# Kernel tuning notes

Measured on AMD Instinct MI355X. Metric: run time of the kernel, lower is better.

Reference implementation:

```python
import jax, jax.numpy as jnp
import numpy as np

B, S, V, D, H = 8, 256, 32000, 1024, 1024
NLAY_H, NLAY_L, HEADS = 2, 2, 8
RATIO, N_LOW, N_HIGH = 4, 16, 4
HD = H // HEADS


def setup_inputs():
    key = jax.random.key(0)
    ks = jax.random.split(key, 16)
    s = 0.02
    f = lambda k, shape: (jax.random.normal(k, shape) * s).astype(jnp.float32)
    return {
        "input_ids": jax.random.randint(ks[0], (B, S), 0, V),
        "emb": f(ks[1], (V, D)),
        "pos": f(ks[2], (S, D)),
        "Wih_h": f(ks[3], (NLAY_H, 3 * H, H)),
        "bih_h": jnp.zeros((NLAY_H, 3 * H), jnp.float32),
        "Whh_h": f(ks[4], (NLAY_H, 3 * H, H)),
        "bhh_h": jnp.zeros((NLAY_H, 3 * H), jnp.float32),
        "Win": f(ks[5], (H, 2 * H)),
        "bin_": jnp.zeros((H,), jnp.float32),
        "Wq": f(ks[6], (H, H)),
        "Wk": f(ks[7], (H, H)),
        "Wv": f(ks[8], (H, H)),
        "Wo": f(ks[9], (H, H)),
        "Wih_l": f(ks[10], (NLAY_L, 3 * H, H)),
        "bih_l": jnp.zeros((NLAY_L, 3 * H), jnp.float32),
        "Whh_l": f(ks[11], (NLAY_L, 3 * H, H)),
        "bhh_l": jnp.zeros((NLAY_L, 3 * H), jnp.float32),
        "ln_g": jnp.ones((H,), jnp.float32),
        "ln_b": jnp.zeros((H,), jnp.float32),
        "Wout": f(ks[12], (V, H)),
    }


def gru_cell(x, h, Wih, bih, Whh, bhh):
    gx = x @ Wih.T + bih  # [B, 3H]
    gh = h @ Whh.T + bhh
    xr, xz, xn = jnp.split(gx, 3, axis=-1)
    hr, hz, hn = jnp.split(gh, 3, axis=-1)
    r = jax.nn.sigmoid(xr + hr)
    z = jax.nn.sigmoid(xz + hz)
    n = jnp.tanh(xn + r * hn)
    return (1.0 - z) * n + z * h


def _forward(input_ids, emb, pos, Wih_h, bih_h, Whh_h, bhh_h, Win, bin_,
             Wq, Wk, Wv, Wo, Wih_l, bih_l, Whh_l, bhh_l, ln_g, ln_b, Wout):
    embeds = emb[input_ids] + pos[None, :S]  # [B, S, D]
    inv_sqrt_hd = np.float32(1.0 / np.sqrt(HD))

    def high_mod(x, hs):  # hs: [NLAY_H, B, H]
        new = []
        for l in range(NLAY_H):
            x = gru_cell(x, hs[l], Wih_h[l], bih_h[l], Whh_h[l], bhh_h[l])
            new.append(x)
        return jnp.stack(new), x

    def low_mod(x, high_cur, hist, mask, ls):
        # input projection over [embed ; current high state]
        inp = jax.nn.gelu(jnp.concatenate([x, high_cur], axis=-1) @ Win.T + bin_)  # [B, H]
        # multi-head cross-attention over high-state history (causal in high steps)
        q = (inp @ Wq.T).reshape(B, HEADS, HD)
        k = (hist @ Wk.T).reshape(B, N_HIGH, HEADS, HD)
        v = (hist @ Wv.T).reshape(B, N_HIGH, HEADS, HD)
        scores = jnp.einsum('bhd,bthd->bht', q, k) * inv_sqrt_hd
        scores = jnp.where(mask[None, None, :], scores, jnp.float32(-1e9))
        attn = jax.nn.softmax(scores, axis=-1)
        ctx = jnp.einsum('bht,bthd->bhd', attn, v).reshape(B, H) @ Wo.T
        x2 = inp + ctx
        new = []
        for l in range(NLAY_L):
            x2 = gru_cell(x2, ls[l], Wih_l[l], bih_l[l], Whh_l[l], bhh_l[l])
            new.append(x2)
        return jnp.stack(new), x2

    def step(carry, t):
        hs_all, ls_all, hist = carry
        e = embeds[:, t]  # [B, D]
        low_step = t % N_LOW
        high_step = low_step // RATIO
        do_high = (low_step % RATIO) == 0
        hs = hs_all[high_step]
        new_hs, high_out = high_mod(e, hs)
        hs_all = hs_all.at[high_step].set(jnp.where(do_high, new_hs, hs))
        hist = hist.at[:, high_step].set(jnp.where(do_high, high_out, hist[:, high_step]))
        mask = jnp.arange(N_HIGH) <= high_step
        ls = ls_all[low_step]
        new_ls, low_out = low_mod(e, hist[:, high_step], hist, mask, ls)
        ls_all = ls_all.at[low_step].set(new_ls)
        mu = low_out.mean(axis=-1, keepdims=True)
        var = ((low_out - mu) ** 2).mean(axis=-1, keepdims=True)
        y = (low_out - mu) / jnp.sqrt(var + 1e-5) * ln_g + ln_b
        return (hs_all, ls_all, hist), y @ Wout.T  # [B, V]

    hs0 = jnp.zeros((N_HIGH, NLAY_H, B, H), jnp.float32)
    ls0 = jnp.zeros((N_LOW, NLAY_L, B, H), jnp.float32)
    hist0 = jnp.zeros((B, N_HIGH, H), jnp.float32)
    _, logits = jax.lax.scan(step, (hs0, ls0, hist0), jnp.arange(S))
    return jnp.transpose(logits, (1, 0, 2))  # [B, S, V]


def reference(input_ids, emb, pos, Wih_h, bih_h, Whh_h, bhh_h, Win, bin_,
              Wq, Wk, Wv, Wo, Wih_l, bih_l, Whh_l, bhh_l, ln_g, ln_b, Wout):
    return _forward(input_ids, emb, pos, Wih_h, bih_h, Whh_h, bhh_h, Win, bin_,
                    Wq, Wk, Wv, Wo, Wih_l, bih_l, Whh_l, bhh_l, ln_g, ln_b, Wout)
```

## Files before the change

kernel.cpp:

```cpp
#include <hip/hip_runtime.h>

typedef unsigned short u16;
typedef float f32x4 __attribute__((ext_vector_type(4)));
typedef __bf16 bf16x8 __attribute__((ext_vector_type(8)));
typedef u16 u16x8 __attribute__((ext_vector_type(8)));

#define DEVFN __device__ __forceinline__


DEVFN u16 f2bf(float f) {
  unsigned u = __builtin_bit_cast(unsigned, f);
  unsigned r = u + 0x7FFFu + ((u >> 16) & 1u);
  return (u16)(r >> 16);
}

DEVFN bf16x8 cvt8(const float* p) {
  float4 f0 = *reinterpret_cast<const float4*>(p);
  float4 f1 = *reinterpret_cast<const float4*>(p + 4);
  u16x8 u;
  u[0] = f2bf(f0.x); u[1] = f2bf(f0.y); u[2] = f2bf(f0.z); u[3] = f2bf(f0.w);
  u[4] = f2bf(f1.x); u[5] = f2bf(f1.y); u[6] = f2bf(f1.z); u[7] = f2bf(f1.w);
  return __builtin_bit_cast(bf16x8, u);
}

DEVFN bf16x8 ldbf(const u16* p) { return *reinterpret_cast<const bf16x8*>(p); }
DEVFN float sigm(float x) { return 1.f / (1.f + expf(-x)); }

DEVFN void gload16(const u16* g, u16* l) {
  __builtin_amdgcn_global_load_lds(
      (const __attribute__((address_space(1))) void*)g,
      (__attribute__((address_space(3))) void*)l, 16, 0, 0);
}

template<int NTSTORE, int OUTF, int BF16OUT, int CADD>
__global__ __launch_bounds__(256) void gemm_lds(
    const u16* __restrict__ A, const u16* __restrict__ W,
    const float* __restrict__ Cadd,
    float* __restrict__ OUT, u16* __restrict__ OUTbf,
    int ldo, int mtiles) {
  __shared__ u16 smA[2][128 * 32];
  __shared__ u16 smB[2][128 * 32];

  int nwg = gridDim.x;
  int orig = blockIdx.x;
  int q = nwg >> 3, r = nwg & 7;
  int xcd = orig & 7, idx = orig >> 3;
  int wg = (xcd < r ? xcd * (q + 1) : r * (q + 1) + (xcd - r) * q) + idx;
  int m0 = (wg % mtiles) * 128;
  int n0 = (wg / mtiles) * 128;

  int tid = threadIdx.x;
  int wv = tid >> 6, lane = tid & 63;
  int lrow = lane >> 2;
  int gcol = ((lane & 3) ^ (lrow & 3)) << 3;

  const u16* gA0 = A + (size_t)(m0 + wv * 32 + lrow) * 1024 + gcol;
  const u16* gB0 = W + (size_t)(n0 + wv * 32 + lrow) * 1024 + gcol;
  u16* lA0 = &smA[0][(wv * 32) * 32];
  u16* lA1 = &smA[0][(wv * 32 + 16) * 32];
  u16* lB0 = &smB[0][(wv * 32) * 32];
  u16* lB1 = &smB[0][(wv * 32 + 16) * 32];
  const int BUFO = 128 * 32;

  f32x4 acc[4][4];
#pragma unroll
  for (int mi = 0; mi < 4; ++mi)
#pragma unroll
    for (int ni = 0; ni < 4; ++ni) acc[mi][ni] = f32x4{0.f, 0.f, 0.f, 0.f};

  int qm = (wv >> 1) * 64, qn = (wv & 1) * 64;
  int lr = lane & 15;
  int kk = (lane >> 4) << 3;

  gload16(gA0, lA0);
  gload16(gA0 + 16 * 1024, lA1);
  gload16(gB0, lB0);
  gload16(gB0 + 16 * 1024, lB1);

  for (int kt = 0; kt < 32; ++kt) {
    int buf = kt & 1;
    __syncthreads();
    if (kt < 31) {
      int k0 = (kt + 1) << 5;
      int bo = (buf ^ 1) * BUFO;
      gload16(gA0 + k0, lA0 + bo);
      gload16(gA0 + 16 * 1024 + k0, lA1 + bo);
      gload16(gB0 + k0, lB0 + bo);
      gload16(gB0 + 16 * 1024 + k0, lB1 + bo);
    }
    bf16x8 av[4], bv[4];
#pragma unroll
    for (int i = 0; i < 4; ++i) {
      int ra = qm + i * 16 + lr;
      av[i] = *(const bf16x8*)&smA[buf][ra * 32 + (kk ^ ((ra & 3) << 3))];
      int rbw = qn + i * 16 + lr;
      bv[i] = *(const bf16x8*)&smB[buf][rbw * 32 + (kk ^ ((rbw & 3) << 3))];
    }
#pragma unroll
    for (int mi = 0; mi < 4; ++mi)
#pragma unroll
      for (int ni = 0; ni < 4; ++ni)
        acc[mi][ni] = __builtin_amdgcn_mfma_f32_16x16x32_bf16(av[mi], bv[ni], acc[mi][ni], 0, 0, 0);
  }

  int rb = (lane >> 4) << 2;
#pragma unroll
  for (int mi = 0; mi < 4; ++mi)
#pragma unroll
    for (int ni = 0; ni < 4; ++ni)
#pragma unroll
      for (int rr = 0; rr < 4; ++rr) {
        int row = m0 + qm + mi * 16 + rb + rr;
        int col = n0 + qn + ni * 16 + lr;
        size_t o = (size_t)row * (size_t)ldo + col;
        float v = acc[mi][ni][rr];
        if constexpr (CADD) v += Cadd[o];
        if constexpr (OUTF) {
          if constexpr (NTSTORE) __builtin_nontemporal_store(v, &OUT[o]);
          else OUT[o] = v;
        }
        if constexpr (BF16OUT) OUTbf[o] = f2bf(v);
      }
}

template<int MT, int NT, int KW>
__global__ __launch_bounds__(64 * KW) void gemm2(
    const u16* __restrict__ A, int lda,
    const void* __restrict__ Wp, int ldw, int kwoff, int wbf,
    const float* __restrict__ Cadd, int ldc,
    float* __restrict__ OUT, u16* __restrict__ OUTbf, int ldo, int K) {
  int tid = threadIdx.x;
  int kw = tid >> 6;
  int lane = tid & 63;
  int lr = lane & 15;
  int kk = (lane >> 4) << 3;
  int n0 = blockIdx.x * (16 * NT);
  int m0 = blockIdx.y * (16 * MT);
  int KP = K / KW;
  int kb = kw * KP + kk;

  f32x4 acc[MT][NT];
#pragma unroll
  for (int mi = 0; mi < MT; ++mi)
#pragma unroll
    for (int ni = 0; ni < NT; ++ni) acc[mi][ni] = f32x4{0.f, 0.f, 0.f, 0.f};

  const u16* ap[MT];
#pragma unroll
  for (int mi = 0; mi < MT; ++mi) ap[mi] = A + (size_t)(m0 + mi * 16 + lr) * (size_t)lda + kb;

  if (wbf) {
    const u16* wb[NT];
#pragma unroll
    for (int ni = 0; ni < NT; ++ni)
      wb[ni] = (const u16*)Wp + (size_t)(n0 + ni * 16 + lr) * (size_t)ldw + kwoff + kb;
    for (int k0 = 0; k0 < KP; k0 += 32) {
      bf16x8 wv[NT];
#pragma unroll
      for (int ni = 0; ni < NT; ++ni) wv[ni] = ldbf(wb[ni] + k0);
#pragma unroll
      for (int mi = 0; mi < MT; ++mi) {
        bf16x8 a = ldbf(ap[mi] + k0);
#pragma unroll
        for (int ni = 0; ni < NT; ++ni)
          acc[mi][ni] = __builtin_amdgcn_mfma_f32_16x16x32_bf16(a, wv[ni], acc[mi][ni], 0, 0, 0);
      }
    }
  } else {
    const float* wf[NT];
#pragma unroll
    for (int ni = 0; ni < NT; ++ni)
      wf[ni] = (const float*)Wp + (size_t)(n0 + ni * 16 + lr) * (size_t)ldw + kwoff + kb;
    for (int k0 = 0; k0 < KP; k0 += 32) {
      bf16x8 wv[NT];
#pragma unroll
      for (int ni = 0; ni < NT; ++ni) wv[ni] = cvt8(wf[ni] + k0);
#pragma unroll
      for (int mi = 0; mi < MT; ++mi) {
        bf16x8 a = ldbf(ap[mi] + k0);
#pragma unroll
        for (int ni = 0; ni < NT; ++ni)
          acc[mi][ni] = __builtin_amdgcn_mfma_f32_16x16x32_bf16(a, wv[ni], acc[mi][ni], 0, 0, 0);
      }
    }
  }

  if constexpr (KW > 1) {
    __shared__ f32x4 red[KW][MT * NT][64];
#pragma unroll
    for (int mi = 0; mi < MT; ++mi)
#pragma unroll
      for (int ni = 0; ni < NT; ++ni) red[kw][mi * NT + ni][lane] = acc[mi][ni];
    __syncthreads();
    if (kw) return;
    for (int w2 = 1; w2 < KW; ++w2)
#pragma unroll
      for (int mi = 0; mi < MT; ++mi)
#pragma unroll
        for (int ni = 0; ni < NT; ++ni) acc[mi][ni] += red[w2][mi * NT + ni][lane];
  }

  int rb = (lane >> 4) << 2;
#pragma unroll
  for (int mi = 0; mi < MT; ++mi)
#pragma unroll
    for (int ni = 0; ni < NT; ++ni)
#pragma unroll
      for (int rr = 0; rr < 4; ++rr) {
        int row = m0 + mi * 16 + rb + rr;
        int col = n0 + ni * 16 + lr;
        size_t o = (size_t)row * (size_t)ldo + col;
        float v = acc[mi][ni][rr];
        if (Cadd) v += Cadd[(size_t)row * (size_t)ldc + col];
        if (OUT) OUT[o] = v;
        if (OUTbf) OUTbf[o] = f2bf(v);
      }
}

struct GruP {
  const u16* X; const u16* Hb; const float* Hf;
  const u16* Wbih; const u16* Wbhh;
  const float* Wfih; const float* Wfhh;
  const float* bih; const float* bhh;
  float* Hof; u16* Hob; u16* hist;
};

__global__ __launch_bounds__(256) void gru_dual(GruP pa, GruP pb, int tiles1, int wbf) {
  GruP p; int m0;
  if ((int)blockIdx.y < tiles1) { p = pa; m0 = blockIdx.y * 32; }
  else { p = pb; m0 = ((int)blockIdx.y - tiles1) * 32; }
  int tid = threadIdx.x;
  int kw = tid >> 6;
  int lane = tid & 63;
  int lr = lane & 15;
  int kk = (lane >> 4) << 3;
  int j0 = blockIdx.x * 16;
  const int KP = 256;
  int kb = kw * KP + kk;

  f32x4 aR[2], aZ[2], aNX[2], aNH[2];
#pragma unroll
  for (int mi = 0; mi < 2; ++mi) {
    aR[mi] = f32x4{0.f, 0.f, 0.f, 0.f};
    aZ[mi] = f32x4{0.f, 0.f, 0.f, 0.f};
    aNX[mi] = f32x4{0.f, 0.f, 0.f, 0.f};
    aNH[mi] = f32x4{0.f, 0.f, 0.f, 0.f};
  }

  const u16* xp[2];
  const u16* hp[2];
#pragma unroll
  for (int mi = 0; mi < 2; ++mi) {
    size_t ro = (size_t)(m0 + mi * 16 + lr) * 1024 + kb;
    xp[mi] = p.X + ro;
    hp[mi] = p.Hb + ro;
  }

  size_t wro = (size_t)(j0 + lr) * 1024 + kb;
  if (wbf) {
    const u16 *pxr = p.Wbih + wro, *pxz = p.Wbih + wro + 1048576, *pxn = p.Wbih + wro + 2097152;
    const u16 *phr = p.Wbhh + wro, *phz = p.Wbhh + wro + 1048576, *phn = p.Wbhh + wro + 2097152;
    for (int k0 = 0; k0 < KP; k0 += 32) {
      bf16x8 wxr = ldbf(pxr + k0), wxz = ldbf(pxz + k0), wxn = ldbf(pxn + k0);
      bf16x8 whr = ldbf(phr + k0), whz = ldbf(phz + k0), whn = ldbf(phn + k0);
#pragma unroll
      for (int mi = 0; mi < 2; ++mi) {
        bf16x8 ax = ldbf(xp[mi] + k0);
        bf16x8 ah = ldbf(hp[mi] + k0);
        aR[mi] = __builtin_amdgcn_mfma_f32_16x16x32_bf16(ax, wxr, aR[mi], 0, 0, 0);
        aR[mi] = __builtin_amdgcn_mfma_f32_16x16x32_bf16(ah, whr, aR[mi], 0, 0, 0);
        aZ[mi] = __builtin_amdgcn_mfma_f32_16x16x32_bf16(ax, wxz, aZ[mi], 0, 0, 0);
        aZ[mi] = __builtin_amdgcn_mfma_f32_16x16x32_bf16(ah, whz, aZ[mi], 0, 0, 0);
        aNX[mi] = __builtin_amdgcn_mfma_f32_16x16x32_bf16(ax, wxn, aNX[mi], 0, 0, 0);
        aNH[mi] = __builtin_amdgcn_mfma_f32_16x16x32_bf16(ah, whn, aNH[mi], 0, 0, 0);
      }
    }
  } else {
    const float *pxr = p.Wfih + wro, *pxz = p.Wfih + wro + 1048576, *pxn = p.Wfih + wro + 2097152;
    const float *phr = p.Wfhh + wro, *phz = p.Wfhh + wro + 1048576, *phn = p.Wfhh + wro + 2097152;
    for (int k0 = 0; k0 < KP; k0 += 32) {
      bf16x8 wxr = cvt8(pxr + k0), wxz = cvt8(pxz + k0), wxn = cvt8(pxn + k0);
      bf16x8 whr = cvt8(phr + k0), whz = cvt8(phz + k0), whn = cvt8(phn + k0);
#pragma unroll
      for (int mi = 0; mi < 2; ++mi) {
        bf16x8 ax = ldbf(xp[mi] + k0);
        bf16x8 ah = ldbf(hp[mi] + k0);
        aR[mi] = __builtin_amdgcn_mfma_f32_16x16x32_bf16(ax, wxr, aR[mi], 0, 0, 0);
        aR[mi] = __builtin_amdgcn_mfma_f32_16x16x32_bf16(ah, whr, aR[mi], 0, 0, 0);
        aZ[mi] = __builtin_amdgcn_mfma_f32_16x16x32_bf16(ax, wxz, aZ[mi], 0, 0, 0);
        aZ[mi] = __builtin_amdgcn_mfma_f32_16x16x32_bf16(ah, whz, aZ[mi], 0, 0, 0);
        aNX[mi] = __builtin_amdgcn_mfma_f32_16x16x32_bf16(ax, wxn, aNX[mi], 0, 0, 0);
        aNH[mi] = __builtin_amdgcn_mfma_f32_16x16x32_bf16(ah, whn, aNH[mi], 0, 0, 0);
      }
    }
  }

  {
    __shared__ f32x4 red[4][8][64];
#pragma unroll
    for (int mi = 0; mi < 2; ++mi) {
      red[kw][mi * 4 + 0][lane] = aR[mi];
      red[kw][mi * 4 + 1][lane] = aZ[mi];
      red[kw][mi * 4 + 2][lane] = aNX[mi];
      red[kw][mi * 4 + 3][lane] = aNH[mi];
    }
    __syncthreads();
    if (kw) return;
    for (int w2 = 1; w2 < 4; ++w2)
#pragma unroll
      for (int mi = 0; mi < 2; ++mi) {
        aR[mi] += red[w2][mi * 4 + 0][lane];
        aZ[mi] += red[w2][mi * 4 + 1][lane];
        aNX[mi] += red[w2][mi * 4 + 2][lane];
        aNH[mi] += red[w2][mi * 4 + 3][lane];
      }
  }

  int c = j0 + lr;
  float br = p.bih[c] + p.bhh[c];
  float bz = p.bih[1024 + c] + p.bhh[1024 + c];
  float bnx = p.bih[2048 + c];
  float bnh = p.bhh[2048 + c];
  int rb = (lane >> 4) << 2;
#pragma unroll
  for (int mi = 0; mi < 2; ++mi)
#pragma unroll
    for (int rr = 0; rr < 4; ++rr) {
      int row = m0 + mi * 16 + rb + rr;
      float r = sigm(aR[mi][rr] + br);
      float z = sigm(aZ[mi][rr] + bz);
      float n = tanhf(aNX[mi][rr] + bnx + r * (aNH[mi][rr] + bnh));
      size_t o = (size_t)row * 1024 + c;
      float hv = (1.f - z) * n + z * p.Hf[o];
      p.Hof[o] = hv;
      u16 hb = f2bf(hv);
      p.Hob[o] = hb;
      if (p.hist) p.hist[o] = hb;
    }
}

__global__ __launch_bounds__(256) void gemm_big(const u16* __restrict__ A,
                                                const void* __restrict__ Wp, int wbf,
                                                float* __restrict__ OUT) {
  int wv = threadIdx.x >> 6;
  int lane = threadIdx.x & 63;
  int lr = lane & 15;
  int kk = (lane >> 4) << 3;
  int m0 = blockIdx.x * 256 + wv * 64;
  int n0 = blockIdx.y * 64;

  f32x4 acc[4][4];
#pragma unroll
  for (int mi = 0; mi < 4; ++mi)
#pragma unroll
    for (int ni = 0; ni < 4; ++ni) acc[mi][ni] = f32x4{0.f, 0.f, 0.f, 0.f};

  const u16* ap[4];
#pragma unroll
  for (int mi = 0; mi < 4; ++mi) ap[mi] = A + (size_t)(m0 + mi * 16 + lr) * 1024 + kk;

  const float* wf[4];
#pragma unroll
  for (int ni = 0; ni < 4; ++ni) wf[ni] = (const float*)Wp + (size_t)(n0 + ni * 16 + lr) * 1024 + kk;
  for (int k0 = 0; k0 < 1024; k0 += 32) {
    bf16x8 wvv[4];
#pragma unroll
    for (int ni = 0; ni < 4; ++ni) wvv[ni] = cvt8(wf[ni] + k0);
#pragma unroll
    for (int mi = 0; mi < 4; ++mi) {
      bf16x8 a = ldbf(ap[mi] + k0);
#pragma unroll
      for (int ni = 0; ni < 4; ++ni)
        acc[mi][ni] = __builtin_amdgcn_mfma_f32_16x16x32_bf16(a, wvv[ni], acc[mi][ni], 0, 0, 0);
    }
  }

  int rb = (lane >> 4) << 2;
#pragma unroll
  for (int mi = 0; mi < 4; ++mi)
#pragma unroll
    for (int ni = 0; ni < 4; ++ni)
#pragma unroll
      for (int rr = 0; rr < 4; ++rr) {
        size_t o = (size_t)(m0 + mi * 16 + rb + rr) * 32000 + (size_t)(n0 + ni * 16 + lr);
        __builtin_nontemporal_store(acc[mi][ni][rr], &OUT[o]);
      }
}

__global__ void cvt_w(const float* __restrict__ src, int src_ld, int col_off,
                      u16* __restrict__ dst, int log2c) {
  size_t idx = ((size_t)blockIdx.x * 256 + threadIdx.x) * 8;
  size_t row = idx >> log2c;
  int col = (int)(idx & ((1u << log2c) - 1));
  const float* s = src + row * (size_t)src_ld + col_off + col;
  *reinterpret_cast<u16x8*>(dst + idx) = __builtin_bit_cast(u16x8, cvt8(s));
}

__global__ void embed_kernel(const int* __restrict__ ids, const float* __restrict__ emb,
                             const float* __restrict__ pos, u16* __restrict__ out) {
  int idx = blockIdx.x * 256 + threadIdx.x;
  int e8 = (idx & 127) << 3;
  int rb = idx >> 7;
  int t = rb >> 3, b = rb & 7;
  int w = t >> 4, lsp = t & 15, g = lsp >> 2, o = lsp & 3;
  int R = ((w << 4) + (o << 2) + g) * 8 + b;
  int tok = ids[b * 256 + t];
  const float* ep = emb + (size_t)tok * 1024 + e8;
  const float* pp = pos + (size_t)t * 1024 + e8;
  u16x8 u;
#pragma unroll
  for (int i = 0; i < 8; ++i) u[i] = f2bf(ep[i] + pp[i]);
  *reinterpret_cast<u16x8*>(out + (size_t)R * 1024 + e8) = u;
}

__global__ void inp_all(const float* __restrict__ einp, const float* __restrict__ kvhAll,
                        const float* __restrict__ bin, float* __restrict__ inpb,
                        u16* __restrict__ inpbf) {
  int idx = blockIdx.x * 256 + threadIdx.x;
  int r = idx >> 10, j = idx & 1023;
  int w = r >> 7, r7 = r & 127;
  int g = (r7 >> 3) & 3, b = r7 & 7;
  float x = einp[idx] + kvhAll[(size_t)(w * 32 + g * 8 + b) * 3072 + 2048 + j] + bin[j];
  float t = tanhf(0.7978845608028654f * (x + 0.044715f * x * x * x));
  float v = 0.5f * x * (1.f + t);
  inpb[idx] = v;
  inpbf[idx] = f2bf(v);
}

__global__ void attn_all(const float* __restrict__ qb, const float* __restrict__ kvhAll,
                         u16* __restrict__ ctxbf) {
  int r = blockIdx.x;
  int w = r >> 7, r7 = r & 127;
  int sp = r7 >> 3;
  int g = sp & 3;
  int b = r7 & 7;
  int lane = threadIdx.x;
  const float* kvb = kvhAll + (size_t)w * 32 * 3072;
  __shared__ float aw[8][4];
  if (lane < 32) {
    int head = lane >> 2, t = lane & 3;
    float s = 0.f;
    if (t <= g) {
      const float* qp = qb + (size_t)r * 1024 + head * 128;
      const float* kp = kvb + (size_t)(t * 8 + b) * 3072 + head * 128;
      for (int d = 0; d < 128; ++d) s += qp[d] * kp[d];
      s *= 0.08838834764831845f;
    }
    float sc[4];
    sc[0] = __shfl(s, (head << 2) + 0);
    sc[1] = __shfl(s, (head << 2) + 1);
    sc[2] = __shfl(s, (head << 2) + 2);
    sc[3] = __shfl(s, (head << 2) + 3);
    if (t == 0) {
      float mx = -1e30f;
      for (int u = 0; u <= g; ++u) mx = fmaxf(mx, sc[u]);
      float p[4] = {0.f, 0.f, 0.f, 0.f};
      float den = 0.f;
      for (int u = 0; u <= g; ++u) { p[u] = expf(sc[u] - mx); den += p[u]; }
      float inv = 1.f / den;
      for (int u = 0; u < 4; ++u) aw[head][u] = (u <= g) ? p[u] * inv : 0.f;
    }
  }
  __syncthreads();
  for (int idx = lane; idx < 1024; idx += 64) {
    int head = idx >> 7;
    float acc = 0.f;
#pragma unroll
    for (int t = 0; t < 4; ++t) acc += aw[head][t] * kvb[(size_t)(t * 8 + b) * 3072 + 1024 + idx];
    ctxbf[(size_t)r * 1024 + idx] = f2bf(acc);
  }
}

__global__ void ln_all(const float* __restrict__ ls1f, const float* __restrict__ g_,
                       const float* __restrict__ b_, u16* __restrict__ Ybf) {
  int bid = blockIdx.x;
  int w = bid >> 7, r7 = bid & 127;
  int tid = threadIdx.x;
  const float* x = ls1f + (size_t)(w + 1) * 131072 + (size_t)r7 * 1024;
  float s = 0.f, s2 = 0.f;
  for (int j = tid; j < 1024; j += 256) { float v = x[j]; s += v; s2 += v * v; }
  for (int off = 32; off; off >>= 1) { s += __shfl_xor(s, off); s2 += __shfl_xor(s2, off); }
  __shared__ float rs[4], rs2[4], mv[2];
  int wv = tid >> 6;
  if ((tid & 63) == 0) { rs[wv] = s; rs2[wv] = s2; }
  __syncthreads();
  if (tid == 0) {
    float S = rs[0] + rs[1] + rs[2] + rs[3];
    float S2 = rs2[0] + rs2[1] + rs2[2] + rs2[3];
    float mu = S * (1.f / 1024.f);
    float var = S2 * (1.f / 1024.f) - mu * mu;
    mv[0] = mu;
    mv[1] = rsqrtf(var + 1e-5f);
  }
  __syncthreads();
  float mu = mv[0], rstd = mv[1];
  int sp = r7 >> 3, b = r7 & 7;
  int g = sp & 3, o = sp >> 2;
  int t = w * 16 + g * 4 + o;
  u16* yrow = Ybf + (size_t)(b * 256 + t) * 1024;
  for (int j = tid; j < 1024; j += 256) {
    float v = (x[j] - mu) * rstd * g_[j] + b_[j];
    yrow[j] = f2bf(v);
  }
}

extern "C" void kernel_launch(void* const* d_in, const int* in_sizes, int n_in,
                              void* d_out, int out_size, void* d_ws, size_t ws_size,
                              hipStream_t stream) {
  const int* ids = (const int*)d_in[0];
  const float* emb = (const float*)d_in[1];
  const float* pos = (const float*)d_in[2];
  const float* Wih_h = (const float*)d_in[3];
  const float* bih_h = (const float*)d_in[4];
  const float* Whh_h = (const float*)d_in[5];
  const float* bhh_h = (const float*)d_in[6];
  const float* Win = (const float*)d_in[7];
  const float* bin_ = (const float*)d_in[8];
  const float* Wq = (const float*)d_in[9];
  const float* Wk = (const float*)d_in[10];
  const float* Wv = (const float*)d_in[11];
  const float* Wo = (const float*)d_in[12];
  const float* Wih_l = (const float*)d_in[13];
  const float* bih_l = (const float*)d_in[14];
  const float* Whh_l = (const float*)d_in[15];
  const float* bhh_l = (const float*)d_in[16];
  const float* ln_g = (const float*)d_in[17];
  const float* ln_b = (const float*)d_in[18];
  const float* Wout = (const float*)d_in[19];
  float* out = (float*)d_out;

  size_t off = 0;
  char* wsb = (char*)d_ws;
  auto allocF = [&](size_t n) { float* p = (float*)(wsb + off); off += n * 4; return p; };
  auto allocU = [&](size_t n) { u16* p = (u16*)(wsb + off); off += n * 2; return p; };

  float* hs0f = allocF((size_t)17 * 32768);
  float* hs1f = allocF((size_t)17 * 32768);
  float* ls0f = allocF((size_t)17 * 131072);
  float* ls1f = allocF((size_t)17 * 131072);
  u16* hs0b = allocU((size_t)17 * 32768);
  u16* hs1b = allocU((size_t)17 * 32768);
  u16* ls0b = allocU((size_t)17 * 131072);
  u16* ls1b = allocU((size_t)17 * 131072);
  u16* histAll = allocU(524288);
  u16* embB = allocU(2097152);
  float* einp = allocF(2097152);
  float* kvhAll = allocF((size_t)512 * 3072);
  float* inpb = allocF(2097152);
  u16* inpbf = allocU(2097152);
  float* qb = allocF(2097152);
  u16* ctxbf = allocU(2097152);
  u16* x2bf = allocU(2097152);
  u16* Ybf = allocU(2097152);

  const size_t WPACK_BYTES = (size_t)(4 * 6291456 + 1048576 + 1048576 + 1048576 + 3145728) * 2;
  bool packW = (off + WPACK_BYTES <= ws_size);
  u16 *WihHb = nullptr, *WhhHb = nullptr, *WihLb = nullptr, *WhhLb = nullptr;
  u16 *WinB0 = nullptr, *WqB = nullptr, *WoB = nullptr, *KVp = nullptr;
  if (packW) {
    WihHb = allocU(6291456);
    WhhHb = allocU(6291456);
    WihLb = allocU(6291456);
    WhhLb = allocU(6291456);
    WinB0 = allocU(1048576);
    WqB = allocU(1048576);
    WoB = allocU(1048576);
    KVp = allocU(3145728);
  }
  bool packWout = packW && (off + (size_t)32768000 * 2 <= ws_size);
  u16* WoutB = nullptr;
  if (packWout) WoutB = allocU(32768000);

  (void)hipMemsetAsync(hs0f, 0, 32768 * 4, stream);
  (void)hipMemsetAsync(hs1f, 0, 32768 * 4, stream);
  (void)hipMemsetAsync(ls0f, 0, 131072 * 4, stream);
  (void)hipMemsetAsync(ls1f, 0, 131072 * 4, stream);
  (void)hipMemsetAsync(hs0b, 0, 32768 * 2, stream);
  (void)hipMemsetAsync(hs1b, 0, 32768 * 2, stream);
  (void)hipMemsetAsync(ls0b, 0, 131072 * 2, stream);
  (void)hipMemsetAsync(ls1b, 0, 131072 * 2, stream);

  embed_kernel<<<1024, 256, 0, stream>>>(ids, emb, pos, embB);
  if (packW) {
    cvt_w<<<3072, 256, 0, stream>>>(Wih_h, 1024, 0, WihHb, 10);
    cvt_w<<<3072, 256, 0, stream>>>(Whh_h, 1024, 0, WhhHb, 10);
    cvt_w<<<3072, 256, 0, stream>>>(Wih_l, 1024, 0, WihLb, 10);
    cvt_w<<<3072, 256, 0, stream>>>(Whh_l, 1024, 0, WhhLb, 10);
    cvt_w<<<512, 256, 0, stream>>>(Win, 2048, 0, WinB0, 10);
    cvt_w<<<512, 256, 0, stream>>>(Wq, 1024, 0, WqB, 10);
    cvt_w<<<512, 256, 0, stream>>>(Wo, 1024, 0, WoB, 10);
    cvt_w<<<512, 256, 0, stream>>>(Wk, 1024, 0, KVp, 10);
    cvt_w<<<512, 256, 0, stream>>>(Wv, 1024, 0, KVp + 1048576, 10);
    cvt_w<<<512, 256, 0, stream>>>(Win, 2048, 1024, KVp + 2097152, 10);
  }
  if (packWout) cvt_w<<<16000, 256, 0, stream>>>(Wout, 1024, 0, WoutB, 10);
  int wbfW = packW ? 1 : 0;

  if (packW)
    gemm_lds<0, 1, 0, 0><<<128, 256, 0, stream>>>(embB, WinB0, nullptr, einp, nullptr, 1024, 16);
  else
    gemm2<2, 2, 2><<<dim3(32, 64), 128, 0, stream>>>(
        embB, 1024, Win, 2048, 0, 0, nullptr, 0, einp, nullptr, 1024, 1024);

  const size_t LW = (size_t)3072 * 1024;
  auto HP = [&](int layer, int w) {
    GruP p;
    if (layer == 0) {
      p.X = embB + (size_t)w * 131072;
      p.Hb = hs0b + (size_t)w * 32768; p.Hf = hs0f + (size_t)w * 32768;
      p.Wbih = WihHb; p.Wbhh = WhhHb; p.Wfih = Wih_h; p.Wfhh = Whh_h;
      p.bih = bih_h; p.bhh = bhh_h;
      p.Hof = hs0f + (size_t)(w + 1) * 32768; p.Hob = hs0b + (size_t)(w + 1) * 32768;
      p.hist = nullptr;
    } else {
      p.X = hs0b + (size_t)(w + 1) * 32768;
      p.Hb = hs1b + (size_t)w * 32768; p.Hf = hs1f + (size_t)w * 32768;
      p.Wbih = WihHb ? WihHb + LW : nullptr; p.Wbhh = WhhHb ? WhhHb + LW : nullptr;
      p.Wfih = Wih_h + LW; p.Wfhh = Whh_h + LW;
      p.bih = bih_h + 3072; p.bhh = bhh_h + 3072;
      p.Hof = hs1f + (size_t)(w + 1) * 32768; p.Hob = hs1b + (size_t)(w + 1) * 32768;
      p.hist = histAll + (size_t)w * 32768;
    }
    return p;
  };
  auto LP = [&](int layer, int w) {
    GruP p;
    if (layer == 0) {
      p.X = x2bf + (size_t)w * 131072;
      p.Hb = ls0b + (size_t)w * 131072; p.Hf = ls0f + (size_t)w * 131072;
      p.Wbih = WihLb; p.Wbhh = WhhLb; p.Wfih = Wih_l; p.Wfhh = Whh_l;
      p.bih = bih_l; p.bhh = bhh_l;
      p.Hof = ls0f + (size_t)(w + 1) * 131072; p.Hob = ls0b + (size_t)(w + 1) * 131072;
      p.hist = nullptr;
    } else {
      p.X = ls0b + (size_t)(w + 1) * 131072;
      p.Hb = ls1b + (size_t)w * 131072; p.Hf = ls1f + (size_t)w * 131072;
      p.Wbih = WihLb ? WihLb + LW : nullptr; p.Wbhh = WhhLb ? WhhLb + LW : nullptr;
      p.Wfih = Wih_l + LW; p.Wfhh = Whh_l + LW;
      p.bih = bih_l + 3072; p.bhh = bhh_l + 3072;
      p.Hof = ls1f + (size_t)(w + 1) * 131072; p.Hob = ls1b + (size_t)(w + 1) * 131072;
      p.hist = nullptr;
    }
    return p;
  };

  gru_dual<<<dim3(64, 1), 256, 0, stream>>>(HP(0, 0), HP(0, 0), 1, wbfW);
  for (int d = 1; d <= 15; ++d)
    gru_dual<<<dim3(64, 2), 256, 0, stream>>>(HP(1, d - 1), HP(0, d), 1, wbfW);
  gru_dual<<<dim3(64, 1), 256, 0, stream>>>(HP(1, 15), HP(1, 15), 1, wbfW);

  if (packW) {
    gemm_lds<0, 1, 0, 0><<<96, 256, 0, stream>>>(histAll, KVp, nullptr, kvhAll, nullptr, 3072, 4);
  } else {
    gemm2<2, 2, 2><<<dim3(32, 16), 128, 0, stream>>>(
        histAll, 1024, Wk, 1024, 0, 0, nullptr, 0, kvhAll, nullptr, 3072, 1024);
    gemm2<2, 2, 2><<<dim3(32, 16), 128, 0, stream>>>(
        histAll, 1024, Wv, 1024, 0, 0, nullptr, 0, kvhAll + 1024, nullptr, 3072, 1024);
    gemm2<2, 2, 2><<<dim3(32, 16), 128, 0, stream>>>(
        histAll, 1024, Win, 2048, 1024, 0, nullptr, 0, kvhAll + 2048, nullptr, 3072, 1024);
  }
  inp_all<<<8192, 256, 0, stream>>>(einp, kvhAll, bin_, inpb, inpbf);
  if (packW)
    gemm_lds<0, 1, 0, 0><<<128, 256, 0, stream>>>(inpbf, WqB, nullptr, qb, nullptr, 1024, 16);
  else
    gemm2<2, 2, 2><<<dim3(32, 64), 128, 0, stream>>>(
        inpbf, 1024, Wq, 1024, 0, 0, nullptr, 0, qb, nullptr, 1024, 1024);
  attn_all<<<2048, 64, 0, stream>>>(qb, kvhAll, ctxbf);
  if (packW)
    gemm_lds<0, 0, 1, 1><<<128, 256, 0, stream>>>(ctxbf, WoB, inpb, nullptr, x2bf, 1024, 16);
  else
    gemm2<2, 2, 2><<<dim3(32, 64), 128, 0, stream>>>(
        ctxbf, 1024, Wo, 1024, 0, 0, inpb, 1024, nullptr, x2bf, 1024, 1024);

  gru_dual<<<dim3(64, 4), 256, 0, stream>>>(LP(0, 0), LP(0, 0), 4, wbfW);
  for (int d = 1; d <= 15; ++d)
    gru_dual<<<dim3(64, 8), 256, 0, stream>>>(LP(1, d - 1), LP(0, d), 4, wbfW);
  gru_dual<<<dim3(64, 4), 256, 0, stream>>>(LP(1, 15), LP(1, 15), 4, wbfW);

  ln_all<<<2048, 256, 0, stream>>>(ls1f, ln_g, ln_b, Ybf);
  if (packWout)
    gemm_lds<1, 1, 0, 0><<<4000, 256, 0, stream>>>(Ybf, WoutB, nullptr, out, nullptr, 32000, 16);
  else
    gemm_big<<<dim3(8, 500), 256, 0, stream>>>(Ybf, Wout, 0, out);
}
```

Measured before the change: 1.109 ms.

## Merge weight conversion launches into one kernel and retune GEMM LDS swizzle

Replaces eleven separate fp32-to-bf16 weight conversion launches with a single segmented kernel that finds its segment from the block index, removing per-launch overhead and tail gaps. Separately, the LDS tile swizzle in the bf16 GEMM now XORs on row bits 1-2 instead of 0-1, and the per-iteration shared-memory read offsets are precomputed outside the k-loop. The swizzle change is meant to reduce LDS bank conflicts on the fragment reads. The segment search adds a small serial loop per block.

Measured after the change: 1.081 ms. 2.5% less time.

```diff
diff --git a/kernel.cpp b/kernel.cpp
--- a/kernel.cpp
+++ b/kernel.cpp
@@ -52,10 +52,10 @@
   int tid = threadIdx.x;
   int wv = tid >> 6, lane = tid & 63;
   int lrow = lane >> 2;
-  int gcol = ((lane & 3) ^ (lrow & 3)) << 3;
-
-  const u16* gA0 = A + (size_t)(m0 + wv * 32 + lrow) * 1024 + gcol;
-  const u16* gB0 = W + (size_t)(n0 + wv * 32 + lrow) * 1024 + gcol;
+  int gcol = ((lane & 3) ^ ((lrow >> 1) & 3)) << 3;
+
+  const u16* gA = A + (size_t)(m0 + wv * 32 + lrow) * 1024 + gcol;
+  const u16* gB = W + (size_t)(n0 + wv * 32 + lrow) * 1024 + gcol;
   u16* lA0 = &smA[0][(wv * 32) * 32];
   u16* lA1 = &smA[0][(wv * 32 + 16) * 32];
   u16* lB0 = &smB[0][(wv * 32) * 32];
@@ -72,10 +72,21 @@
   int lr = lane & 15;
   int kk = (lane >> 4) << 3;
 
-  gload16(gA0, lA0);
-  gload16(gA0 + 16 * 1024, lA1);
-  gload16(gB0, lB0);
-  gload16(gB0 + 16 * 1024, lB1);
+  int offA[4], offB[4];
+#pragma unroll
+  for (int i = 0; i < 4; ++i) {
+    int ra = qm + i * 16 + lr;
+    offA[i] = ra * 64 + ((kk ^ (((ra >> 1) & 3) << 3)) << 1);
+    int rbw = qn + i * 16 + lr;
+    offB[i] = rbw * 64 + ((kk ^ (((rbw >> 1) & 3) << 3)) << 1);
+  }
+  const char* baseA = (const char*)&smA[0][0];
+  const char* baseB = (const char*)&smB[0][0];
+
+  gload16(gA, lA0);
+  gload16(gA + 16 * 1024, lA1);
+  gload16(gB, lB0);
+  gload16(gB + 16 * 1024, lB1);
 
   for (int kt = 0; kt < 32; ++kt) {
     int buf = kt & 1;
@@ -83,18 +94,17 @@
     if (kt < 31) {
       int k0 = (kt + 1) << 5;
       int bo = (buf ^ 1) * BUFO;
-      gload16(gA0 + k0, lA0 + bo);
-      gload16(gA0 + 16 * 1024 + k0, lA1 + bo);
-      gload16(gB0 + k0, lB0 + bo);
-      gload16(gB0 + 16 * 1024 + k0, lB1 + bo);
-    }
+      gload16(gA + k0, lA0 + bo);
+      gload16(gA + 16 * 1024 + k0, lA1 + bo);
+      gload16(gB + k0, lB0 + bo);
+      gload16(gB + 16 * 1024 + k0, lB1 + bo);
+    }
+    int bb = buf * (BUFO * 2);
     bf16x8 av[4], bv[4];
 #pragma unroll
     for (int i = 0; i < 4; ++i) {
-      int ra = qm + i * 16 + lr;
-      av[i] = *(const bf16x8*)&smA[buf][ra * 32 + (kk ^ ((ra & 3) << 3))];
-      int rbw = qn + i * 16 + lr;
-      bv[i] = *(const bf16x8*)&smB[buf][rbw * 32 + (kk ^ ((rbw & 3) << 3))];
+      av[i] = *(const bf16x8*)(baseA + bb + offA[i]);
+      bv[i] = *(const bf16x8*)(baseB + bb + offB[i]);
     }
 #pragma unroll
     for (int mi = 0; mi < 4; ++mi)
@@ -387,13 +397,19 @@
       }
 }
 
-__global__ void cvt_w(const float* __restrict__ src, int src_ld, int col_off,
-                      u16* __restrict__ dst, int log2c) {
-  size_t idx = ((size_t)blockIdx.x * 256 + threadIdx.x) * 8;
-  size_t row = idx >> log2c;
-  int col = (int)(idx & ((1u << log2c) - 1));
-  const float* s = src + row * (size_t)src_ld + col_off + col;
-  *reinterpret_cast<u16x8*>(dst + idx) = __builtin_bit_cast(u16x8, cvt8(s));
+struct CvtSeg { const float* src; u16* dst; int src_ld; int col_off; int log2c; int nblk; };
+struct CvtArgs { CvtSeg seg[11]; int nseg; };
+
+__global__ void cvt_all(CvtArgs a) {
+  int blk = blockIdx.x;
+  int s = 0;
+  while (s < a.nseg - 1 && blk >= a.seg[s].nblk) { blk -= a.seg[s].nblk; ++s; }
+  const CvtSeg g = a.seg[s];
+  size_t idx = ((size_t)blk * 256 + threadIdx.x) * 8;
+  size_t row = idx >> g.log2c;
+  int col = (int)(idx & ((1u << g.log2c) - 1));
+  const float* sp = g.src + row * (size_t)g.src_ld + g.col_off + col;
+  *reinterpret_cast<u16x8*>(g.dst + idx) = __builtin_bit_cast(u16x8, cvt8(sp));
 }
 
 __global__ void embed_kernel(const int* __restrict__ ids, const float* __restrict__ emb,
@@ -582,18 +598,27 @@
 
   embed_kernel<<<1024, 256, 0, stream>>>(ids, emb, pos, embB);
   if (packW) {
-    cvt_w<<<3072, 256, 0, stream>>>(Wih_h, 1024, 0, WihHb, 10);
-    cvt_w<<<3072, 256, 0, stream>>>(Whh_h, 1024, 0, WhhHb, 10);
-    cvt_w<<<3072, 256, 0, stream>>>(Wih_l, 1024, 0, WihLb, 10);
-    cvt_w<<<3072, 256, 0, stream>>>(Whh_l, 1024, 0, WhhLb, 10);
-    cvt_w<<<512, 256, 0, stream>>>(Win, 2048, 0, WinB0, 10);
-    cvt_w<<<512, 256, 0, stream>>>(Wq, 1024, 0, WqB, 10);
-    cvt_w<<<512, 256, 0, stream>>>(Wo, 1024, 0, WoB, 10);
-    cvt_w<<<512, 256, 0, stream>>>(Wk, 1024, 0, KVp, 10);
-    cvt_w<<<512, 256, 0, stream>>>(Wv, 1024, 0, KVp + 1048576, 10);
-    cvt_w<<<512, 256, 0, stream>>>(Win, 2048, 1024, KVp + 2097152, 10);
-  }
-  if (packWout) cvt_w<<<16000, 256, 0, stream>>>(Wout, 1024, 0, WoutB, 10);
+    CvtArgs ca{};
+    int ns = 0, tot = 0;
+    auto add = [&](const float* s, u16* d, int ld, int co, int l2c, size_t nelem) {
+      int nb = (int)(nelem / 2048);
+      ca.seg[ns++] = CvtSeg{s, d, ld, co, l2c, nb};
+      tot += nb;
+    };
+    add(Wih_h, WihHb, 1024, 0, 10, 6291456);
+    add(Whh_h, WhhHb, 1024, 0, 10, 6291456);
+    add(Wih_l, WihLb, 1024, 0, 10, 6291456);
+    add(Whh_l, WhhLb, 1024, 0, 10, 6291456);
+    add(Win, WinB0, 2048, 0, 10, 1048576);
+    add(Wq, WqB, 1024, 0, 10, 1048576);
+    add(Wo, WoB, 1024, 0, 10, 1048576);
+    add(Wk, KVp, 1024, 0, 10, 1048576);
+    add(Wv, KVp + 1048576, 1024, 0, 10, 1048576);
+    add(Win, KVp + 2097152, 2048, 1024, 10, 1048576);
+    if (packWout) add(Wout, WoutB, 1024, 0, 10, 32768000);
+    ca.nseg = ns;
+    cvt_all<<<tot, 256, 0, stream>>>(ca);
+  }
   int wbfW = packW ? 1 : 0;
 
   if (packW)
```
